# Kernel tuning notes

Measured on AMD Instinct MI355X. Metric: run time of the kernel, lower is better.

## Reference

```python
import jax, jax.numpy as jnp
import numpy as np

N = 100000      # nodes
E = 640000      # edges
V_IN = 128
U_IN = 64
HID = 128
B = 128         # graphs


def setup_inputs() -> dict:
    key = jax.random.key(0)
    ks = jax.random.split(key, 9)
    x = jax.random.normal(ks[0], (N, V_IN), dtype=jnp.float32)
    edge_index = jax.random.randint(ks[1], (2, E), 0, N, dtype=jnp.int64)
    edge_attr = jax.random.normal(ks[2], (E, HID), dtype=jnp.float32)
    u = jax.random.normal(ks[3], (B, U_IN), dtype=jnp.float32)
    batch = jnp.sort(jax.random.randint(ks[4], (N,), 0, B, dtype=jnp.int64))
    fan_in1 = V_IN + HID + U_IN
    W1 = jax.random.normal(ks[5], (fan_in1, HID), dtype=jnp.float32) / np.sqrt(fan_in1)
    b1 = jnp.zeros((HID,), dtype=jnp.float32)
    W2 = jax.random.normal(ks[6], (HID, HID), dtype=jnp.float32) / np.sqrt(HID)
    b2 = jnp.zeros((HID,), dtype=jnp.float32)
    return {"x": x, "edge_index": edge_index, "edge_attr": edge_attr, "u": u,
            "batch": batch, "W1": W1, "b1": b1, "W2": W2, "b2": b2}


def reference(x, edge_index, edge_attr, u, batch, W1, b1, W2, b2):
    col = edge_index[1]
    # scatter_add edge_attr into destination-node slots: [N, HID]
    agg = jax.ops.segment_sum(edge_attr, col, num_segments=x.shape[0])
    # concat [x, agg, u[batch]] -> [N, V_IN + HID + U_IN]
    h = jnp.concatenate([x, agg, u[batch]], axis=1)
    h = jax.nn.relu(h @ W1 + b1)
    return h @ W2 + b2
```

## Files before the change

### kernel.cpp

```cpp
#include <hip/hip_runtime.h>
#include <hip/hip_bf16.h>

#define V_IN 128
#define U_IN 64
#define HID 128
#define K1  (V_IN + HID + U_IN)

typedef __attribute__((ext_vector_type(8))) short bf16x8;
typedef __attribute__((ext_vector_type(4))) float f32x4;

static __device__ __forceinline__ unsigned short f2bf(float f) {
    __hip_bfloat16 h = __float2bfloat16(f);
    union { __hip_bfloat16 h; unsigned short u; } v; v.h = h;
    return v.u;
}
static __device__ __forceinline__ unsigned int f2bf2(float lo, float hi) {
    __hip_bfloat162 h2 = __float22bfloat162_rn(make_float2(lo, hi));
    union { __hip_bfloat162 h; unsigned int u; } v; v.h = h2;
    return v.u;
}

__global__ __launch_bounds__(256) void zero_kernel(int* __restrict__ p, int n)
{
    int i = blockIdx.x * 256 + threadIdx.x;
    if (i < n) p[i] = 0;
}


__global__ __launch_bounds__(256) void hist_kernel(
    const int* __restrict__ col, int* __restrict__ deg, int E)
{
    int e = blockIdx.x * 256 + threadIdx.x;
    if (e < E) atomicAdd(&deg[col[e]], 1);
}

__global__ __launch_bounds__(256) void scan_partial(
    const int* __restrict__ deg, int* __restrict__ blockSums, int N)
{
    __shared__ int sdata[256];
    int base = blockIdx.x * 1024;
    int tid  = threadIdx.x;
    int s = 0;
    #pragma unroll
    for (int j = 0; j < 4; ++j) {
        int i = base + tid * 4 + j;
        if (i < N) s += deg[i];
    }
    sdata[tid] = s;
    __syncthreads();
    for (int off = 128; off > 0; off >>= 1) {
        if (tid < off) sdata[tid] += sdata[tid + off];
        __syncthreads();
    }
    if (tid == 0) blockSums[blockIdx.x] = sdata[0];
}

__global__ __launch_bounds__(1024) void scan_blocksums(
    int* __restrict__ blockSums, int NB)
{
    __shared__ int s[1024];
    int tid = threadIdx.x;
    int v = (tid < NB) ? blockSums[tid] : 0;
    s[tid] = v;
    __syncthreads();
    for (int off = 1; off < 1024; off <<= 1) {
        int t = (tid >= off) ? s[tid - off] : 0;
        __syncthreads();
        s[tid] += t;
        __syncthreads();
    }
    if (tid < NB) blockSums[tid] = s[tid] - v;
}

__global__ __launch_bounds__(256) void scan_final(
    const int* __restrict__ deg, const int* __restrict__ blockSums,
    int* __restrict__ offsets, int* __restrict__ cur, int N, int E)
{
    __shared__ int sdata[256];
    int base = blockIdx.x * 1024;
    int tid  = threadIdx.x;
    int loc[4];
    int s = 0;
    #pragma unroll
    for (int j = 0; j < 4; ++j) {
        int i = base + tid * 4 + j;
        loc[j] = (i < N) ? deg[i] : 0;
        s += loc[j];
    }
    int mine = s;
    sdata[tid] = s;
    __syncthreads();
    for (int off = 1; off < 256; off <<= 1) {
        int t = (tid >= off) ? sdata[tid - off] : 0;
        __syncthreads();
        sdata[tid] += t;
        __syncthreads();
    }
    int prefix = blockSums[blockIdx.x] + sdata[tid] - mine;
    #pragma unroll
    for (int j = 0; j < 4; ++j) {
        int i = base + tid * 4 + j;
        if (i < N) { offsets[i] = prefix; cur[i] = prefix; prefix += loc[j]; }
    }
    if (blockIdx.x == 0 && tid == 0) offsets[N] = E;
}

__global__ __launch_bounds__(256) void fill_kernel(
    const int* __restrict__ col, int* __restrict__ cur,
    int* __restrict__ eidx, int E)
{
    int e = blockIdx.x * 256 + threadIdx.x;
    if (e < E) {
        int p = atomicAdd(&cur[col[e]], 1);
        eidx[p] = e;
    }
}

__global__ __launch_bounds__(256) void prep_w(
    const float* __restrict__ W1, const float* __restrict__ W2,
    unsigned short* __restrict__ Wt1, unsigned short* __restrict__ Wt2)
{
    int id = blockIdx.x * 256 + threadIdx.x;
    if (id < HID * K1) {
        int c = id / K1, k = id - c * K1;
        Wt1[id] = f2bf(W1[(size_t)k * HID + c]);
    }
    if (id < HID * HID) {
        int c = id >> 7, k = id & 127;
        Wt2[id] = f2bf(W2[(size_t)k * HID + c]);
    }
}

#define ROWS 32
#define LDA_E 328
#define LDH_E 136
#define ECAP 1280

__global__ __launch_bounds__(512, 4) void mlp_mfma(
    const float* __restrict__ x,
    const float* __restrict__ edge_attr,
    const int*   __restrict__ offsets,
    const int*   __restrict__ eidx,
    const float* __restrict__ u,
    const int*   __restrict__ batch,
    const unsigned short* __restrict__ Wt1,
    const unsigned short* __restrict__ Wt2,
    const float* __restrict__ b1, const float* __restrict__ b2,
    float* __restrict__ out, int N)
{
    __shared__ __align__(16) unsigned short A[ROWS * LDA_E];
    __shared__ __align__(16) unsigned short H[ROWS * LDH_E];
    __shared__ int Eidx[ECAP];
    const int tid  = threadIdx.x;
    const int n0   = blockIdx.x * ROWS;
    const int lane = tid & 63;
    const int wave = tid >> 6;
    const int l15  = lane & 15;
    const int lhi  = lane >> 4;
    const int wcol = wave * 16 + l15;

    const int nEnd   = (n0 + ROWS < N) ? n0 + ROWS : N;
    const int s_base = offsets[n0];
    const int s_end  = offsets[nEnd];
    const int cnt    = (s_end - s_base < ECAP) ? s_end - s_base : ECAP;
    for (int i = tid; i < cnt; i += 512) Eidx[i] = eidx[s_base + i];

    #pragma unroll
    for (int it = 0; it < 3; ++it) {
        int t   = tid + it * 512;
        int row = t / 48;
        int s   = t - row * 48;
        int n   = n0 + row;
        unsigned short* Arow = &A[row * LDA_E];
        float4 v = make_float4(0.f, 0.f, 0.f, 0.f);
        int colbase;
        if (s < 32) {
            if (n < N) v = ((const float4*)(x + (size_t)n * V_IN))[s];
            colbase = s * 4;
        } else {
            if (n < N) {
                int b = batch[n];
                v = ((const float4*)(u + (size_t)b * U_IN))[s - 32];
            }
            colbase = V_IN + HID + (s - 32) * 4;
        }
        uint2 o; o.x = f2bf2(v.x, v.y); o.y = f2bf2(v.z, v.w);
        *(uint2*)&Arow[colbase] = o;
    }
    __syncthreads();

    #pragma unroll
    for (int it = 0; it < 2; ++it) {
        int t   = tid + it * 512;
        int row = t >> 5;
        int c   = t & 31;
        int n   = n0 + row;
        f32x4 a0 = {0.f, 0.f, 0.f, 0.f};
        f32x4 a1 = {0.f, 0.f, 0.f, 0.f};
        f32x4 a2 = {0.f, 0.f, 0.f, 0.f};
        f32x4 a3 = {0.f, 0.f, 0.f, 0.f};
        if (n < N) {
            int ls = offsets[n]     - s_base;
            int le = offsets[n + 1] - s_base;
            int j = ls;
            for (; j + 3 < le; j += 4) {
                int e0, e1, e2, e3;
                if (j + 3 < ECAP) {
                    e0 = Eidx[j];     e1 = Eidx[j + 1];
                    e2 = Eidx[j + 2]; e3 = Eidx[j + 3];
                } else {
                    e0 = eidx[s_base + j];     e1 = eidx[s_base + j + 1];
                    e2 = eidx[s_base + j + 2]; e3 = eidx[s_base + j + 3];
                }
                f32x4 v0 = __builtin_nontemporal_load((const f32x4*)(edge_attr + (size_t)e0 * HID) + c);
                f32x4 v1 = __builtin_nontemporal_load((const f32x4*)(edge_attr + (size_t)e1 * HID) + c);
                f32x4 v2 = __builtin_nontemporal_load((const f32x4*)(edge_attr + (size_t)e2 * HID) + c);
                f32x4 v3 = __builtin_nontemporal_load((const f32x4*)(edge_attr + (size_t)e3 * HID) + c);
                a0 += v0; a1 += v1; a2 += v2; a3 += v3;
            }
            for (; j < le; ++j) {
                int e0 = (j < ECAP) ? Eidx[j] : eidx[s_base + j];
                a0 += __builtin_nontemporal_load((const f32x4*)(edge_attr + (size_t)e0 * HID) + c);
            }
        }
        f32x4 asum = (a0 + a1) + (a2 + a3);
        uint2 o;
        o.x = f2bf2(asum[0], asum[1]);
        o.y = f2bf2(asum[2], asum[3]);
        *(uint2*)&A[row * LDA_E + V_IN + c * 4] = o;
    }

    bf16x8 w1f[10], w2f[4];
    #pragma unroll
    for (int ks = 0; ks < 10; ++ks)
        w1f[ks] = *(const bf16x8*)(Wt1 + (size_t)wcol * K1 + ks * 32 + lhi * 8);
    #pragma unroll
    for (int ks = 0; ks < 4; ++ks)
        w2f[ks] = *(const bf16x8*)(Wt2 + (size_t)wcol * HID + ks * 32 + lhi * 8);
    const float b1v = b1[wcol];
    const float b2v = b2[wcol];

    __syncthreads();

    f32x4 acc[2] = {{0.f, 0.f, 0.f, 0.f}, {0.f, 0.f, 0.f, 0.f}};
    #pragma unroll
    for (int ks = 0; ks < 10; ++ks) {
        #pragma unroll
        for (int h = 0; h < 2; ++h) {
            bf16x8 af = *(const bf16x8*)&A[(h * 16 + l15) * LDA_E + ks * 32 + lhi * 8];
            acc[h] = __builtin_amdgcn_mfma_f32_16x16x32_bf16(af, w1f[ks], acc[h], 0, 0, 0);
        }
    }
    #pragma unroll
    for (int h = 0; h < 2; ++h)
        #pragma unroll
        for (int r = 0; r < 4; ++r) {
            float hv = fmaxf(acc[h][r] + b1v, 0.f);
            H[(h * 16 + lhi * 4 + r) * LDH_E + wcol] = f2bf(hv);
        }
    __syncthreads();

    f32x4 acc2[2] = {{0.f, 0.f, 0.f, 0.f}, {0.f, 0.f, 0.f, 0.f}};
    #pragma unroll
    for (int ks = 0; ks < 4; ++ks) {
        #pragma unroll
        for (int h = 0; h < 2; ++h) {
            bf16x8 hf = *(const bf16x8*)&H[(h * 16 + l15) * LDH_E + ks * 32 + lhi * 8];
            acc2[h] = __builtin_amdgcn_mfma_f32_16x16x32_bf16(hf, w2f[ks], acc2[h], 0, 0, 0);
        }
    }
    #pragma unroll
    for (int h = 0; h < 2; ++h)
        #pragma unroll
        for (int r = 0; r < 4; ++r) {
            int n = n0 + h * 16 + lhi * 4 + r;
            if (n < N) out[(size_t)n * HID + wcol] = acc2[h][r] + b2v;
        }
}

extern "C" void kernel_launch(void* const* d_in, const int* in_sizes, int n_in,
                              void* d_out, int out_size, void* d_ws, size_t ws_size,
                              hipStream_t stream) {
    const float* x          = (const float*)d_in[0];
    const int*   edge_index = (const int*)  d_in[1];
    const float* edge_attr  = (const float*)d_in[2];
    const float* u          = (const float*)d_in[3];
    const int*   batch      = (const int*)  d_in[4];
    const float* W1         = (const float*)d_in[5];
    const float* b1         = (const float*)d_in[6];
    const float* W2         = (const float*)d_in[7];
    const float* b2         = (const float*)d_in[8];
    float* out = (float*)d_out;

    const int N = in_sizes[0] / V_IN;
    const int E = in_sizes[1] / 2;
    const int* col = edge_index + E;

    unsigned short* Wt1  = (unsigned short*)d_ws;
    unsigned short* Wt2  = Wt1 + (size_t)K1 * HID;
    int* deg       = (int*)(Wt2 + (size_t)HID * HID);
    int* cur       = deg + N;
    int* offsets   = cur + N;
    int* blockSums = offsets + N + 1;
    int* eidx      = blockSums + 2048;

    const int NB = (N + 1023) / 1024;

    zero_kernel   <<<(N + 255) / 256, 256, 0, stream>>>(deg, N);
    hist_kernel   <<<(E + 255) / 256, 256, 0, stream>>>(col, deg, E);
    scan_partial  <<<NB, 256, 0, stream>>>(deg, blockSums, N);
    scan_blocksums<<<1, 1024, 0, stream>>>(blockSums, NB);
    scan_final    <<<NB, 256, 0, stream>>>(deg, blockSums, offsets, cur, N, E);
    fill_kernel   <<<(E + 255) / 256, 256, 0, stream>>>(col, cur, eidx, E);
    prep_w        <<<(HID * K1 + 255) / 256, 256, 0, stream>>>(W1, W2, Wt1, Wt2);

    mlp_mfma<<<(N + ROWS - 1) / ROWS, 512, 0, stream>>>(
        x, edge_attr, offsets, eidx, u, batch, Wt1, Wt2, b1, b2, out, N);
}
```

Baseline: 207.7 us.

## Fuse prep kernels, drop blocksum scan launch, unroll gather by eight, nontemporal IO

```diff
diff --git a/kernel.cpp b/kernel.cpp
--- a/kernel.cpp
+++ b/kernel.cpp
@@ -20,10 +20,21 @@
     return v.u;
 }
 
-__global__ __launch_bounds__(256) void zero_kernel(int* __restrict__ p, int n)
-{
-    int i = blockIdx.x * 256 + threadIdx.x;
-    if (i < n) p[i] = 0;
+__global__ __launch_bounds__(256) void zero_prep(
+    const float* __restrict__ W1, const float* __restrict__ W2,
+    unsigned short* __restrict__ Wt1, unsigned short* __restrict__ Wt2,
+    int* __restrict__ deg, int N)
+{
+    int id = blockIdx.x * 256 + threadIdx.x;
+    if (id < N) deg[id] = 0;
+    if (id < HID * K1) {
+        int c = id / K1, k = id - c * K1;
+        Wt1[id] = f2bf(W1[(size_t)k * HID + c]);
+    }
+    if (id < HID * HID) {
+        int c = id >> 7, k = id & 127;
+        Wt2[id] = f2bf(W2[(size_t)k * HID + c]);
+    }
 }
 
 
@@ -55,30 +66,25 @@
     if (tid == 0) blockSums[blockIdx.x] = sdata[0];
 }
 
-__global__ __launch_bounds__(1024) void scan_blocksums(
-    int* __restrict__ blockSums, int NB)
-{
-    __shared__ int s[1024];
-    int tid = threadIdx.x;
-    int v = (tid < NB) ? blockSums[tid] : 0;
-    s[tid] = v;
-    __syncthreads();
-    for (int off = 1; off < 1024; off <<= 1) {
-        int t = (tid >= off) ? s[tid - off] : 0;
-        __syncthreads();
-        s[tid] += t;
-        __syncthreads();
-    }
-    if (tid < NB) blockSums[tid] = s[tid] - v;
-}
-
 __global__ __launch_bounds__(256) void scan_final(
     const int* __restrict__ deg, const int* __restrict__ blockSums,
     int* __restrict__ offsets, int* __restrict__ cur, int N, int E)
 {
     __shared__ int sdata[256];
+    __shared__ int rdata[256];
+    int tid = threadIdx.x;
+
+    int part = 0;
+    for (int i = tid; i < (int)blockIdx.x; i += 256) part += blockSums[i];
+    rdata[tid] = part;
+    __syncthreads();
+    for (int off = 128; off > 0; off >>= 1) {
+        if (tid < off) rdata[tid] += rdata[tid + off];
+        __syncthreads();
+    }
+    const int blockPrefix = rdata[0];
+
     int base = blockIdx.x * 1024;
-    int tid  = threadIdx.x;
     int loc[4];
     int s = 0;
     #pragma unroll
@@ -96,7 +102,7 @@
         sdata[tid] += t;
         __syncthreads();
     }
-    int prefix = blockSums[blockIdx.x] + sdata[tid] - mine;
+    int prefix = blockPrefix + sdata[tid] - mine;
     #pragma unroll
     for (int j = 0; j < 4; ++j) {
         int i = base + tid * 4 + j;
@@ -113,21 +119,6 @@
     if (e < E) {
         int p = atomicAdd(&cur[col[e]], 1);
         eidx[p] = e;
-    }
-}
-
-__global__ __launch_bounds__(256) void prep_w(
-    const float* __restrict__ W1, const float* __restrict__ W2,
-    unsigned short* __restrict__ Wt1, unsigned short* __restrict__ Wt2)
-{
-    int id = blockIdx.x * 256 + threadIdx.x;
-    if (id < HID * K1) {
-        int c = id / K1, k = id - c * K1;
-        Wt1[id] = f2bf(W1[(size_t)k * HID + c]);
-    }
-    if (id < HID * HID) {
-        int c = id >> 7, k = id & 127;
-        Wt2[id] = f2bf(W2[(size_t)k * HID + c]);
     }
 }
 
@@ -172,19 +163,19 @@
         int s   = t - row * 48;
         int n   = n0 + row;
         unsigned short* Arow = &A[row * LDA_E];
-        float4 v = make_float4(0.f, 0.f, 0.f, 0.f);
+        f32x4 v = {0.f, 0.f, 0.f, 0.f};
         int colbase;
         if (s < 32) {
-            if (n < N) v = ((const float4*)(x + (size_t)n * V_IN))[s];
+            if (n < N) v = __builtin_nontemporal_load((const f32x4*)(x + (size_t)n * V_IN) + s);
             colbase = s * 4;
         } else {
             if (n < N) {
                 int b = batch[n];
-                v = ((const float4*)(u + (size_t)b * U_IN))[s - 32];
+                v = *((const f32x4*)(u + (size_t)b * U_IN) + (s - 32));
             }
             colbase = V_IN + HID + (s - 32) * 4;
         }
-        uint2 o; o.x = f2bf2(v.x, v.y); o.y = f2bf2(v.z, v.w);
+        uint2 o; o.x = f2bf2(v[0], v[1]); o.y = f2bf2(v[2], v[3]);
         *(uint2*)&Arow[colbase] = o;
     }
     __syncthreads();
@@ -203,7 +194,31 @@
             int ls = offsets[n]     - s_base;
             int le = offsets[n + 1] - s_base;
             int j = ls;
-            for (; j + 3 < le; j += 4) {
+            for (; j + 7 < le; j += 8) {
+                int e0, e1, e2, e3, e4, e5, e6, e7;
+                if (j + 7 < ECAP) {
+                    e0 = Eidx[j];     e1 = Eidx[j + 1];
+                    e2 = Eidx[j + 2]; e3 = Eidx[j + 3];
+                    e4 = Eidx[j + 4]; e5 = Eidx[j + 5];
+                    e6 = Eidx[j + 6]; e7 = Eidx[j + 7];
+                } else {
+                    e0 = eidx[s_base + j];     e1 = eidx[s_base + j + 1];
+                    e2 = eidx[s_base + j + 2]; e3 = eidx[s_base + j + 3];
+                    e4 = eidx[s_base + j + 4]; e5 = eidx[s_base + j + 5];
+                    e6 = eidx[s_base + j + 6]; e7 = eidx[s_base + j + 7];
+                }
+                f32x4 v0 = __builtin_nontemporal_load((const f32x4*)(edge_attr + (size_t)e0 * HID) + c);
+                f32x4 v1 = __builtin_nontemporal_load((const f32x4*)(edge_attr + (size_t)e1 * HID) + c);
+                f32x4 v2 = __builtin_nontemporal_load((const f32x4*)(edge_attr + (size_t)e2 * HID) + c);
+                f32x4 v3 = __builtin_nontemporal_load((const f32x4*)(edge_attr + (size_t)e3 * HID) + c);
+                f32x4 v4 = __builtin_nontemporal_load((const f32x4*)(edge_attr + (size_t)e4 * HID) + c);
+                f32x4 v5 = __builtin_nontemporal_load((const f32x4*)(edge_attr + (size_t)e5 * HID) + c);
+                f32x4 v6 = __builtin_nontemporal_load((const f32x4*)(edge_attr + (size_t)e6 * HID) + c);
+                f32x4 v7 = __builtin_nontemporal_load((const f32x4*)(edge_attr + (size_t)e7 * HID) + c);
+                a0 += v0; a1 += v1; a2 += v2; a3 += v3;
+                a0 += v4; a1 += v5; a2 += v6; a3 += v7;
+            }
+            if (j + 3 < le) {
                 int e0, e1, e2, e3;
                 if (j + 3 < ECAP) {
                     e0 = Eidx[j];     e1 = Eidx[j + 1];
@@ -217,6 +232,7 @@
                 f32x4 v2 = __builtin_nontemporal_load((const f32x4*)(edge_attr + (size_t)e2 * HID) + c);
                 f32x4 v3 = __builtin_nontemporal_load((const f32x4*)(edge_attr + (size_t)e3 * HID) + c);
                 a0 += v0; a1 += v1; a2 += v2; a3 += v3;
+                j += 4;
             }
             for (; j < le; ++j) {
                 int e0 = (j < ECAP) ? Eidx[j] : eidx[s_base + j];
@@ -230,6 +246,8 @@
         *(uint2*)&A[row * LDA_E + V_IN + c * 4] = o;
     }
 
+    __builtin_amdgcn_sched_barrier(0);
+
     bf16x8 w1f[10], w2f[4];
     #pragma unroll
     for (int ks = 0; ks < 10; ++ks)
@@ -274,7 +292,8 @@
         #pragma unroll
         for (int r = 0; r < 4; ++r) {
             int n = n0 + h * 16 + lhi * 4 + r;
-            if (n < N) out[(size_t)n * HID + wcol] = acc2[h][r] + b2v;
+            if (n < N)
+                __builtin_nontemporal_store(acc2[h][r] + b2v, out + (size_t)n * HID + wcol);
         }
 }
 
@@ -305,14 +324,13 @@
     int* eidx      = blockSums + 2048;
 
     const int NB = (N + 1023) / 1024;
-
-    zero_kernel   <<<(N + 255) / 256, 256, 0, stream>>>(deg, N);
-    hist_kernel   <<<(E + 255) / 256, 256, 0, stream>>>(col, deg, E);
-    scan_partial  <<<NB, 256, 0, stream>>>(deg, blockSums, N);
-    scan_blocksums<<<1, 1024, 0, stream>>>(blockSums, NB);
-    scan_final    <<<NB, 256, 0, stream>>>(deg, blockSums, offsets, cur, N, E);
-    fill_kernel   <<<(E + 255) / 256, 256, 0, stream>>>(col, cur, eidx, E);
-    prep_w        <<<(HID * K1 + 255) / 256, 256, 0, stream>>>(W1, W2, Wt1, Wt2);
+    const int ZP = ((N > HID * K1 ? N : HID * K1) + 255) / 256;
+
+    zero_prep   <<<ZP, 256, 0, stream>>>(W1, W2, Wt1, Wt2, deg, N);
+    hist_kernel <<<(E + 255) / 256, 256, 0, stream>>>(col, deg, E);
+    scan_partial<<<NB, 256, 0, stream>>>(deg, blockSums, N);
+    scan_final  <<<NB, 256, 0, stream>>>(deg, blockSums, offsets, cur, N, E);
+    fill_kernel <<<(E + 255) / 256, 256, 0, stream>>>(col, cur, eidx, E);
 
     mlp_mfma<<<(N + ROWS - 1) / ROWS, 512, 0, stream>>>(
         x, edge_attr, offsets, eidx, u, batch, Wt1, Wt2, b1, b2, out, N);
```

New measurement: 216.1 us. +4.0%, slower.
